# Optimization experiments

Hardware: AMD Instinct MI355X
Metric: run time of the kernel (lower is better)

Reference implementation:

```python
import jax, jax.numpy as jnp
import numpy as np

N_STATES = 512   # N hidden states
M_SYMS   = 256   # M = emission symbols AND sequence length (as in original code)
BATCH    = 256


def setup_inputs() -> dict:
    key = jax.random.key(0)
    k1, k2, k3, k4 = jax.random.split(key, 4)
    return {
        "batch": jax.random.randint(k1, (BATCH, M_SYMS), 0, M_SYMS, dtype=jnp.int32),
        "unnorm_emission": jax.random.normal(k2, (N_STATES, M_SYMS), dtype=jnp.float32),
        "unnorm_transition": jax.random.normal(k3, (N_STATES, N_STATES), dtype=jnp.float32),
        "unnorm_priors": jax.random.normal(k4, (N_STATES,), dtype=jnp.float32),
    }


def reference(batch, unnorm_emission, unnorm_transition, unnorm_priors):
    # log_E[n, m] = log P(obs=m | state=n); softmax over symbols (dim=1 in torch)
    log_E = jax.nn.log_softmax(unnorm_emission, axis=1)          # [N, M]
    # log_T normalized over dim=0 (columns sum to 1), as in torch source
    log_T = jax.nn.log_softmax(unnorm_transition, axis=0)        # [N, N]
    log_priors = jax.nn.log_softmax(unnorm_priors, axis=0)       # [N]

    # emission gather: em[b, t, n] = log_E[n, batch[b, t]]
    em = log_E.T[batch]                                          # [B, T, N]

    alpha0 = em[:, 0, :] + log_priors                            # [B, N]

    def step(alpha, em_t):
        # new_alpha[b, i] = logsumexp_k( log_T[i, k] + alpha[b, k] ) + em_t[b, i]
        new = jax.nn.logsumexp(alpha[:, None, :] + log_T[None, :, :], axis=2) + em_t
        return new, jax.nn.logsumexp(new, axis=1)                # carry, per-step log-sum

    em_rest = jnp.swapaxes(em[:, 1:, :], 0, 1)                   # [T-1, B, N]
    _, lse_rest = jax.lax.scan(step, alpha0, em_rest)            # [T-1, B]

    log_sums = jnp.concatenate(
        [jax.nn.logsumexp(alpha0, axis=1)[:, None], lse_rest.T], axis=1
    )                                                            # [B, T]
    return log_sums
```

## Files before the change

kernel.cpp:

```cpp
#include <hip/hip_runtime.h>
#include <hip/hip_bf16.h>

#define NS 512
#define MS 256
#define TB 256
#define NWG 16
#define BPG 16

#define OFF_EEXP  0u
#define OFF_PEXP  524288u
#define OFF_TFRAG 526336u

typedef __attribute__((ext_vector_type(8))) short short8;
typedef __attribute__((ext_vector_type(4))) float f32x4;

__device__ __forceinline__ unsigned short bf_bits(float f) {
    __hip_bfloat16 h = __float2bfloat16(f);
    unsigned short u; __builtin_memcpy(&u, &h, 2); return u;
}

__global__ void k_emission(const float* __restrict__ E, float* __restrict__ expET) {
    int n = blockIdx.x;
    int lane = threadIdx.x;
    const float* row = E + (size_t)n * MS;
    float v[4]; float mx = -1e30f;
#pragma unroll
    for (int j = 0; j < 4; ++j) { v[j] = row[lane + 64 * j]; mx = fmaxf(mx, v[j]); }
#pragma unroll
    for (int off = 1; off < 64; off <<= 1) mx = fmaxf(mx, __shfl_xor(mx, off));
    float s = 0.f;
#pragma unroll
    for (int j = 0; j < 4; ++j) s += __expf(v[j] - mx);
#pragma unroll
    for (int off = 1; off < 64; off <<= 1) s += __shfl_xor(s, off);
    float lse = mx + __logf(s);
#pragma unroll
    for (int j = 0; j < 4; ++j)
        expET[(size_t)(lane + 64 * j) * NS + n] = __expf(v[j] - lse);
}

__global__ void k_transition(const float* __restrict__ U, __hip_bfloat16* __restrict__ Tf) {
    int k = blockIdx.x;
    int lane = threadIdx.x;
    float v[8]; float mx = -1e30f;
#pragma unroll
    for (int j = 0; j < 8; ++j) { v[j] = U[(size_t)(lane + 64 * j) * NS + k]; mx = fmaxf(mx, v[j]); }
#pragma unroll
    for (int off = 1; off < 64; off <<= 1) mx = fmaxf(mx, __shfl_xor(mx, off));
    float s = 0.f;
#pragma unroll
    for (int j = 0; j < 8; ++j) s += __expf(v[j] - mx);
#pragma unroll
    for (int off = 1; off < 64; off <<= 1) s += __shfl_xor(s, off);
    float lse = mx + __logf(s);
    int kb = k >> 5, hk = (k >> 3) & 3, jj = k & 7;
#pragma unroll
    for (int j = 0; j < 8; ++j) {
        int i = lane + 64 * j;
        int st = i >> 4, li = i & 15;
        size_t byte = ((size_t)(st * 16 + kb) << 10) + (unsigned)(hk * 16 + li) * 16 + jj * 2;
        *reinterpret_cast<unsigned short*>(reinterpret_cast<char*>(Tf) + byte) =
            bf_bits(__expf(v[j] - lse));
    }
}

__global__ void k_priors(const float* __restrict__ U, float* __restrict__ pexp) {
    int lane = threadIdx.x;
    float v[8]; float mx = -1e30f;
#pragma unroll
    for (int j = 0; j < 8; ++j) { v[j] = U[lane + 64 * j]; mx = fmaxf(mx, v[j]); }
#pragma unroll
    for (int off = 1; off < 64; off <<= 1) mx = fmaxf(mx, __shfl_xor(mx, off));
    float s = 0.f;
#pragma unroll
    for (int j = 0; j < 8; ++j) s += __expf(v[j] - mx);
#pragma unroll
    for (int off = 1; off < 64; off <<= 1) s += __shfl_xor(s, off);
    float lse = mx + __logf(s);
#pragma unroll
    for (int j = 0; j < 8; ++j) pexp[lane + 64 * j] = __expf(v[j] - lse);
}

__launch_bounds__(512, 2)
__global__ void k_forward(const int* __restrict__ batch, const float* __restrict__ expET,
                          const __hip_bfloat16* __restrict__ Tf,
                          const float* __restrict__ pexp,
                          float* __restrict__ out) {
    __shared__ __align__(16) char Alds[2][16 * 1024];
    __shared__ __align__(16) char Tlds[8][15 * 1024];
    __shared__ float qred[8][BPG];
    __shared__ float qinv_s[BPG];

    const int tid = threadIdx.x;
    const int lane = tid & 63;
    const int w = tid >> 6;
    const int hi = lane >> 4;
    const int lo = lane & 15;
    const int g = blockIdx.x;
    const int b0 = g * BPG;
    const char* TfC = reinterpret_cast<const char*>(Tf);

#pragma unroll
    for (int c = 49; c < 64; ++c) {
        const int kb = c >> 2, stL = c & 3, st = w * 4 + stL;
        short8 v = *reinterpret_cast<const short8*>(TfC + ((size_t)(st * 16 + kb) << 10) + lane * 16);
        *reinterpret_cast<short8*>(&Tlds[w][(c - 49) * 1024 + lane * 16]) = v;
    }

    {
        int symr[4];
#pragma unroll
        for (int r = 0; r < 4; ++r) symr[r] = batch[(size_t)(b0 + hi * 4 + r) * TB];
        float p[4] = {0.f, 0.f, 0.f, 0.f};
#pragma unroll
        for (int stL = 0; stL < 4; ++stL) {
            int s = w * 64 + stL * 16 + lo;
            float pe = pexp[s];
            const int kbp = w * 2 + (stL >> 1);
            const int hip = (stL & 1) * 2 + (lo >> 3);
#pragma unroll
            for (int r = 0; r < 4; ++r) {
                float a = expET[(size_t)symr[r] * NS + s] * pe;
                p[r] += a;
                *reinterpret_cast<unsigned short*>(
                    &Alds[0][kbp * 1024 + (hip * 16 + hi * 4 + r) * 16 + (lo & 7) * 2]) = bf_bits(a);
            }
        }
#pragma unroll
        for (int off = 1; off < 16; off <<= 1)
#pragma unroll
            for (int r = 0; r < 4; ++r) p[r] += __shfl_xor(p[r], off);
        if (lo == 0)
#pragma unroll
            for (int r = 0; r < 4; ++r) qred[w][hi * 4 + r] = p[r];
    }
    __syncthreads();
    float nrm = 0.f;
    if (tid < BPG) {
        float q = 0.f;
#pragma unroll
        for (int w2 = 0; w2 < 8; ++w2) q += qred[w2][tid];
        float lq = __logf(q);
        nrm = lq;
        out[(size_t)(b0 + tid) * TB] = lq;
        qinv_s[tid] = 1.0f / q;
    }
    __syncthreads();

    short8 tf[49];
#pragma unroll
    for (int c = 0; c < 49; ++c) {
        const int kb = c >> 2, stL = c & 3, st = w * 4 + stL;
        tf[c] = *reinterpret_cast<const short8*>(TfC + ((size_t)(st * 16 + kb) << 10) + lane * 16);
    }

    for (int t = 1; t < TB; ++t) {
        const int pr = (t - 1) & 1, pw = t & 1;

        int symr[4];
#pragma unroll
        for (int r = 0; r < 4; ++r) symr[r] = batch[(size_t)(b0 + hi * 4 + r) * TB + t];
        float qi[4];
#pragma unroll
        for (int r = 0; r < 4; ++r) qi[r] = qinv_s[hi * 4 + r];
        float fac[4][4];
#pragma unroll
        for (int stL = 0; stL < 4; ++stL)
#pragma unroll
            for (int r = 0; r < 4; ++r)
                fac[stL][r] = expET[(size_t)symr[r] * NS + w * 64 + stL * 16 + lo] * qi[r];

        f32x4 acc[4] = {};
        const char* Ab = &Alds[pr][0];
#pragma unroll
        for (int kb = 0; kb < 16; ++kb) {
            short8 af = *reinterpret_cast<const short8*>(Ab + kb * 1024 + lane * 16);
#pragma unroll
            for (int stL = 0; stL < 4; ++stL) {
                const int c = kb * 4 + stL;
                short8 bf;
                if (c < 49) bf = tf[c];
                else bf = *reinterpret_cast<const short8*>(&Tlds[w][(c - 49) * 1024 + lane * 16]);
                acc[stL] = __builtin_amdgcn_mfma_f32_16x16x32_bf16(af, bf, acc[stL], 0, 0, 0);
            }
        }

        float p[4] = {0.f, 0.f, 0.f, 0.f};
#pragma unroll
        for (int stL = 0; stL < 4; ++stL) {
            const int kbp = w * 2 + (stL >> 1);
            const int hip = (stL & 1) * 2 + (lo >> 3);
#pragma unroll
            for (int r = 0; r < 4; ++r) {
                float a = acc[stL][r] * fac[stL][r];
                p[r] += a;
                *reinterpret_cast<unsigned short*>(
                    &Alds[pw][kbp * 1024 + (hip * 16 + hi * 4 + r) * 16 + (lo & 7) * 2]) = bf_bits(a);
            }
        }
#pragma unroll
        for (int off = 1; off < 16; off <<= 1)
#pragma unroll
            for (int r = 0; r < 4; ++r) p[r] += __shfl_xor(p[r], off);
        if (lo == 0)
#pragma unroll
            for (int r = 0; r < 4; ++r) qred[w][hi * 4 + r] = p[r];
        __syncthreads();

        if (tid < BPG) {
            float q = 0.f;
#pragma unroll
            for (int w2 = 0; w2 < 8; ++w2) q += qred[w2][tid];
            float lq = __logf(q);
            nrm += lq;
            out[(size_t)(b0 + tid) * TB + t] = nrm;
            qinv_s[tid] = 1.0f / q;
        }
        __syncthreads();
    }
}

extern "C" void kernel_launch(void* const* d_in, const int* in_sizes, int n_in,
                              void* d_out, int out_size, void* d_ws, size_t ws_size,
                              hipStream_t stream) {
    const int* batch = (const int*)d_in[0];
    const float* unE = (const float*)d_in[1];
    const float* unT = (const float*)d_in[2];
    const float* unP = (const float*)d_in[3];
    float* outp = (float*)d_out;

    char* ws = (char*)d_ws;
    float* expET = (float*)(ws + OFF_EEXP);
    float* pexp = (float*)(ws + OFF_PEXP);
    __hip_bfloat16* Tfrag = (__hip_bfloat16*)(ws + OFF_TFRAG);

    k_emission<<<NS, 64, 0, stream>>>(unE, expET);
    k_transition<<<NS, 64, 0, stream>>>(unT, Tfrag);
    k_priors<<<1, 64, 0, stream>>>(unP, pexp);
    k_forward<<<NWG, 512, 0, stream>>>(batch, expET, Tfrag, pexp, outp);
}
```

Baseline: 645.0 us.

## Double-buffer per-step normalizer and drop second barrier per timestep

Partial row sums now go into a double-buffered shared array laid out [buf][batch][wave]. Every wave reduces the 8 partials redundantly at the start of the next step and broadcasts the reciprocal by shuffle, so each timestep needs one __syncthreads instead of two and the serial single-thread reduction phase is gone. The 49 pinned transition fragments are loaded before the prologue as float vectors behind an asm barrier, which keeps them in registers. The cost is redundant reduction work in all waves, a final-step epilogue, and more register pressure early in the kernel.

```diff
diff --git a/kernel.cpp b/kernel.cpp
--- a/kernel.cpp
+++ b/kernel.cpp
@@ -6,6 +6,7 @@
 #define TB 256
 #define NWG 16
 #define BPG 16
+#define NPIN 49
 
 #define OFF_EEXP  0u
 #define OFF_PEXP  524288u
@@ -88,8 +89,7 @@
                           float* __restrict__ out) {
     __shared__ __align__(16) char Alds[2][16 * 1024];
     __shared__ __align__(16) char Tlds[8][15 * 1024];
-    __shared__ float qred[8][BPG];
-    __shared__ float qinv_s[BPG];
+    __shared__ __align__(16) float qred[2][BPG][8];
 
     const int tid = threadIdx.x;
     const int lane = tid & 63;
@@ -100,11 +100,21 @@
     const int b0 = g * BPG;
     const char* TfC = reinterpret_cast<const char*>(Tf);
 
-#pragma unroll
-    for (int c = 49; c < 64; ++c) {
+    f32x4 tf[NPIN];
+#pragma unroll
+    for (int c = 0; c < NPIN; ++c) {
+        const int kb = c >> 2, stL = c & 3, st = w * 4 + stL;
+        tf[c] = *reinterpret_cast<const f32x4*>(TfC + ((size_t)(st * 16 + kb) << 10) + lane * 16);
+    }
+#pragma unroll
+    for (int c = 0; c < NPIN; ++c)
+        asm volatile("" : "+v"(tf[c]));
+
+#pragma unroll
+    for (int c = NPIN; c < 64; ++c) {
         const int kb = c >> 2, stL = c & 3, st = w * 4 + stL;
         short8 v = *reinterpret_cast<const short8*>(TfC + ((size_t)(st * 16 + kb) << 10) + lane * 16);
-        *reinterpret_cast<short8*>(&Tlds[w][(c - 49) * 1024 + lane * 16]) = v;
+        *reinterpret_cast<short8*>(&Tlds[w][(c - NPIN) * 1024 + lane * 16]) = v;
     }
 
     {
@@ -132,37 +142,30 @@
             for (int r = 0; r < 4; ++r) p[r] += __shfl_xor(p[r], off);
         if (lo == 0)
 #pragma unroll
-            for (int r = 0; r < 4; ++r) qred[w][hi * 4 + r] = p[r];
+            for (int r = 0; r < 4; ++r) qred[0][hi * 4 + r][w] = p[r];
     }
     __syncthreads();
+
     float nrm = 0.f;
-    if (tid < BPG) {
-        float q = 0.f;
-#pragma unroll
-        for (int w2 = 0; w2 < 8; ++w2) q += qred[w2][tid];
-        float lq = __logf(q);
-        nrm = lq;
-        out[(size_t)(b0 + tid) * TB] = lq;
-        qinv_s[tid] = 1.0f / q;
-    }
-    __syncthreads();
-
-    short8 tf[49];
-#pragma unroll
-    for (int c = 0; c < 49; ++c) {
-        const int kb = c >> 2, stL = c & 3, st = w * 4 + stL;
-        tf[c] = *reinterpret_cast<const short8*>(TfC + ((size_t)(st * 16 + kb) << 10) + lane * 16);
-    }
 
     for (int t = 1; t < TB; ++t) {
         const int pr = (t - 1) & 1, pw = t & 1;
 
+        f32x4 qa = *reinterpret_cast<const f32x4*>(&qred[pr][lane & 15][0]);
+        f32x4 qb = *reinterpret_cast<const f32x4*>(&qred[pr][lane & 15][4]);
+        float qv = ((qa[0] + qa[1]) + (qa[2] + qa[3])) + ((qb[0] + qb[1]) + (qb[2] + qb[3]));
+        float qil = 1.0f / qv;
+        if (w == 0) {
+            nrm += __logf(qv);
+            if (lane < 16) out[(size_t)(b0 + lane) * TB + (t - 1)] = nrm;
+        }
+        float qi[4];
+#pragma unroll
+        for (int r = 0; r < 4; ++r) qi[r] = __shfl(qil, hi * 4 + r);
+
         int symr[4];
 #pragma unroll
         for (int r = 0; r < 4; ++r) symr[r] = batch[(size_t)(b0 + hi * 4 + r) * TB + t];
-        float qi[4];
-#pragma unroll
-        for (int r = 0; r < 4; ++r) qi[r] = qinv_s[hi * 4 + r];
         float fac[4][4];
 #pragma unroll
         for (int stL = 0; stL < 4; ++stL)
@@ -179,8 +182,8 @@
             for (int stL = 0; stL < 4; ++stL) {
                 const int c = kb * 4 + stL;
                 short8 bf;
-                if (c < 49) bf = tf[c];
-                else bf = *reinterpret_cast<const short8*>(&Tlds[w][(c - 49) * 1024 + lane * 16]);
+                if (c < NPIN) bf = __builtin_bit_cast(short8, tf[c]);
+                else bf = *reinterpret_cast<const short8*>(&Tlds[w][(c - NPIN) * 1024 + lane * 16]);
                 acc[stL] = __builtin_amdgcn_mfma_f32_16x16x32_bf16(af, bf, acc[stL], 0, 0, 0);
             }
         }
@@ -204,19 +207,16 @@
             for (int r = 0; r < 4; ++r) p[r] += __shfl_xor(p[r], off);
         if (lo == 0)
 #pragma unroll
-            for (int r = 0; r < 4; ++r) qred[w][hi * 4 + r] = p[r];
+            for (int r = 0; r < 4; ++r) qred[pw][hi * 4 + r][w] = p[r];
         __syncthreads();
-
-        if (tid < BPG) {
-            float q = 0.f;
-#pragma unroll
-            for (int w2 = 0; w2 < 8; ++w2) q += qred[w2][tid];
-            float lq = __logf(q);
-            nrm += lq;
-            out[(size_t)(b0 + tid) * TB + t] = nrm;
-            qinv_s[tid] = 1.0f / q;
-        }
-        __syncthreads();
+    }
+
+    if (w == 0) {
+        f32x4 qa = *reinterpret_cast<const f32x4*>(&qred[1][lane & 15][0]);
+        f32x4 qb = *reinterpret_cast<const f32x4*>(&qred[1][lane & 15][4]);
+        float qv = ((qa[0] + qa[1]) + (qa[2] + qa[3])) + ((qb[0] + qb[1]) + (qb[2] + qb[3]));
+        nrm += __logf(qv);
+        if (lane < 16) out[(size_t)(b0 + lane) * TB + 255] = nrm;
     }
 }
 
```

Result: slower. 931.0 us (+44.3%).
